# Performance work log

Measured on AMD Instinct MI355X. Metric: run time of the kernel, lower is better.

Reference implementation:

```python
import jax, jax.numpy as jnp
import numpy as np

N = 50000   # nodes
E = 800000  # edges (avg degree 16)
D = 128     # in = hidden = out feats


def setup_inputs() -> dict:
    key = jax.random.key(0)
    ks = jax.random.split(key, 9)
    x = jax.random.normal(ks[0], (N, D), dtype=jnp.float32)
    edge_index = jax.random.randint(ks[1], (2, E), 0, N, dtype=jnp.int64)
    s = 1.0 / np.sqrt(D)
    # SAGEConv layer 0 (128 -> 128): lin_l (aggregated neighbors, with bias), lin_r (root, no bias)
    Wl0 = jax.random.uniform(ks[2], (D, D), jnp.float32, -s, s)
    Wr0 = jax.random.uniform(ks[3], (D, D), jnp.float32, -s, s)
    b0 = jax.random.uniform(ks[4], (D,), jnp.float32, -s, s)
    # SAGEConv layer 1 (128 -> 128)
    Wl1 = jax.random.uniform(ks[5], (D, D), jnp.float32, -s, s)
    Wr1 = jax.random.uniform(ks[6], (D, D), jnp.float32, -s, s)
    b1 = jax.random.uniform(ks[7], (D,), jnp.float32, -s, s)
    return {"x": x, "edge_index": edge_index,
            "Wl0": Wl0, "Wr0": Wr0, "b0": b0,
            "Wl1": Wl1, "Wr1": Wr1, "b1": b1}


def _sage_conv(x, src, dst, Wl, Wr, b):
    # mean aggregation of neighbor messages x[src] into dst nodes
    msgs = x[src]                                                    # [E, D]
    summed = jax.ops.segment_sum(msgs, dst, num_segments=N)         # [N, D]
    deg = jax.ops.segment_sum(jnp.ones((src.shape[0], 1), x.dtype), dst,
                              num_segments=N)                       # [N, 1]
    agg = summed / jnp.maximum(deg, 1.0)
    # out = lin_l(agg) + lin_r(x); only lin_l has bias (PyG default)
    return agg @ Wl.T + b + x @ Wr.T


def reference(x, edge_index, Wl0, Wr0, b0, Wl1, Wr1, b1):
    src, dst = edge_index[0], edge_index[1]
    h = jax.nn.relu(_sage_conv(x, src, dst, Wl0, Wr0, b0))
    out = _sage_conv(h, src, dst, Wl1, Wr1, b1)  # no ReLU on last layer
    return out
```

## Files before the change

### kernel.cpp

```cpp
#include <hip/hip_runtime.h>


#define D 128
#define NBITS 7
#define BNODES 128
#define GA 64
#define AGGB 2048
typedef unsigned short u16;
typedef unsigned u32;
typedef short bf16x8 __attribute__((ext_vector_type(8)));
typedef float f32x4 __attribute__((ext_vector_type(4)));

__device__ __forceinline__ u16 f2bf(float f) {
    union { float f; unsigned u; } x;
    x.f = f;
    unsigned r = x.u + 0x7FFF + ((x.u >> 16) & 1);
    return (u16)(r >> 16);
}
__device__ __forceinline__ float bf2f(u16 b) {
    union { unsigned u; float f; } x;
    x.u = ((unsigned)b) << 16;
    return x.f;
}

__global__ __launch_bounds__(1024) void hist_and_convert(
        const int* __restrict__ dst, int* __restrict__ Gcounts, int E, int NB, int chunk,
        const float* __restrict__ x, u16* __restrict__ xq, int xOcts, int n32,
        const float* __restrict__ w0, const float* __restrict__ w1,
        const float* __restrict__ w2, const float* __restrict__ w3,
        u16* __restrict__ o0, u16* __restrict__ o1,
        u16* __restrict__ o2, u16* __restrict__ o3) {
    if (blockIdx.x < GA) {
        __shared__ int cnt[512];
        for (int i = threadIdx.x; i < NB; i += 1024) cnt[i] = 0;
        __syncthreads();
        int base = blockIdx.x * chunk;
        int end = base + chunk; if (end > E) end = E;
        for (int e = base + threadIdx.x; e < end; e += 1024)
            atomicAdd(&cnt[dst[e] >> NBITS], 1);
        __syncthreads();
        for (int b = threadIdx.x; b < NB; b += 1024)
            Gcounts[b * GA + blockIdx.x] = cnt[b];
    } else {
        int i = (blockIdx.x - GA) * 1024 + threadIdx.x;
        if (i < xOcts) {
            int node = i >> 4;
            int f = (i & 15) * 8;
            int q = f >> 5, off = f & 31;
            float4 va = *(const float4*)&x[node * D + f];
            float4 vb = *(const float4*)&x[node * D + f + 4];
            bf16x8 o;
            o[0] = (short)f2bf(va.x); o[1] = (short)f2bf(va.y);
            o[2] = (short)f2bf(va.z); o[3] = (short)f2bf(va.w);
            o[4] = (short)f2bf(vb.x); o[5] = (short)f2bf(vb.y);
            o[6] = (short)f2bf(vb.z); o[7] = (short)f2bf(vb.w);
            *(bf16x8*)&xq[q * n32 + node * 32 + off] = o;
        } else {
            int j = i - xOcts;
            const int q = D * D / 4;
            if (j < 4 * q) {
                int m = j / q, k = j % q;
                const float* in = (m == 0) ? w0 : (m == 1) ? w1 : (m == 2) ? w2 : w3;
                u16* op = (m == 0) ? o0 : (m == 1) ? o1 : (m == 2) ? o2 : o3;
                float4 v = *(const float4*)&in[k * 4];
                ushort4 o;
                o.x = f2bf(v.x); o.y = f2bf(v.y); o.z = f2bf(v.z); o.w = f2bf(v.w);
                *(ushort4*)&op[k * 4] = o;
            }
        }
    }
}

__global__ __launch_bounds__(1024) void scan1_kernel(const int* __restrict__ in,
                                                     int* __restrict__ excl,
                                                     int* __restrict__ totals, int n) {
    int chunk = blockIdx.x;
    int i = chunk * 1024 + threadIdx.x;
    int v = (i < n) ? in[i] : 0;
    int lane = threadIdx.x & 63;
    int wid = threadIdx.x >> 6;
    int s = v;
    #pragma unroll
    for (int off = 1; off < 64; off <<= 1) {
        int t = __shfl_up(s, off);
        if (lane >= off) s += t;
    }
    __shared__ int wsum[16];
    if (lane == 63) wsum[wid] = s;
    __syncthreads();
    if (wid == 0) {
        int ws = (lane < 16) ? wsum[lane] : 0;
        #pragma unroll
        for (int off = 1; off < 16; off <<= 1) {
            int t = __shfl_up(ws, off);
            if (lane >= off) ws += t;
        }
        if (lane < 16) wsum[lane] = ws;
    }
    __syncthreads();
    int wave_off = (wid > 0) ? wsum[wid - 1] : 0;
    int incl = s + wave_off;
    if (i < n) excl[i] = incl - v;
    if (threadIdx.x == 1023) totals[chunk] = incl;
}

__device__ __forceinline__ void load_choff(const int* __restrict__ totals,
                                           int nChunks, int* choff) {
    if (threadIdx.x < 64) {
        int t = threadIdx.x;
        int v = (t < nChunks) ? totals[t] : 0;
        int s = v;
        #pragma unroll
        for (int off = 1; off < 64; off <<= 1) {
            int u = __shfl_up(s, off);
            if (t >= off) s += u;
        }
        if (t < 32) choff[t] = s - v;
    }
}

__global__ __launch_bounds__(1024) void bucket_scatter(const int* __restrict__ src,
                                                       const int* __restrict__ dst,
                                                       const int* __restrict__ excl,
                                                       const int* __restrict__ totals,
                                                       u32* __restrict__ Ebuck,
                                                       int E, int NB, int chunk, int nChunks) {
    __shared__ int cur[512];
    __shared__ int choff[32];
    load_choff(totals, nChunks, choff);
    __syncthreads();
    for (int b = threadIdx.x; b < NB; b += 1024) {
        int idx = b * GA + blockIdx.x;
        cur[b] = excl[idx] + choff[idx >> 10];
    }
    __syncthreads();
    int base = blockIdx.x * chunk;
    int end = base + chunk; if (end > E) end = E;
    for (int e = base + threadIdx.x; e < end; e += 1024) {
        int d = dst[e];
        int b = d >> NBITS;
        int pos = atomicAdd(&cur[b], 1);
        Ebuck[pos] = ((u32)(d & (BNODES - 1)) << 16) | (u32)src[e];
    }
}

__global__ __launch_bounds__(256) void bucket_sort_csr(const u32* __restrict__ Ebuck,
                                                       const int* __restrict__ excl_g,
                                                       const int* __restrict__ totals,
                                                       int* __restrict__ row_ptr,
                                                       u16* __restrict__ csr,
                                                       int E, int N, int NB, int nChunks) {
    __shared__ int hist[BNODES], excl[BNODES], cur[BNODES];
    __shared__ u16 sorted[8192];
    __shared__ int choff[32];
    load_choff(totals, nChunks, choff);
    __syncthreads();
    int b = blockIdx.x;
    int idx0 = b * GA;
    int start = excl_g[idx0] + choff[idx0 >> 10];
    int endv = E;
    if (b + 1 < NB) {
        int idx1 = (b + 1) * GA;
        endv = excl_g[idx1] + choff[idx1 >> 10];
    }
    int cnt = endv - start;
    if (cnt > 8192) cnt = 8192;
    for (int i = threadIdx.x; i < BNODES; i += 256) hist[i] = 0;
    __syncthreads();
    for (int i = threadIdx.x; i < cnt; i += 256)
        atomicAdd(&hist[Ebuck[start + i] >> 16], 1);
    __syncthreads();
    if (threadIdx.x == 0) {
        int run = 0;
        for (int i = 0; i < BNODES; ++i) { excl[i] = run; run += hist[i]; }
    }
    __syncthreads();
    for (int i = threadIdx.x; i < BNODES; i += 256) {
        cur[i] = excl[i];
        int g = b * BNODES + i;
        if (g <= N) row_ptr[g] = start + excl[i];
    }
    __syncthreads();
    for (int i = threadIdx.x; i < cnt; i += 256) {
        u32 r = Ebuck[start + i];
        int pos = atomicAdd(&cur[r >> 16], 1);
        sorted[pos] = (u16)(r & 0xFFFF);
    }
    __syncthreads();
    for (int i = threadIdx.x; i < cnt; i += 256)
        csr[start + i] = sorted[i];
}

__global__ __launch_bounds__(256) void aggregate_pin(const u16* __restrict__ xq,
                                                     const int* __restrict__ row_ptr,
                                                     const u16* __restrict__ csr,
                                                     u16* __restrict__ aggq,
                                                     int n, int n32, int chunkN) {
    int b = blockIdx.x;
    int strip = b & 3;
    int cid = (b >> 3) * 2 + ((b >> 2) & 1);
    int slot = (threadIdx.x >> 6) * 16 + ((threadIdx.x & 63) >> 2);
    int fl = (threadIdx.x & 3) * 8;
    const u16* __restrict__ base = xq + strip * n32;
    u16* __restrict__ obase = aggq + strip * n32;
    int start = cid * chunkN;
    int endn = start + chunkN; if (endn > n) endn = n;
    for (int node = start + slot; node < endn; node += 64) {
        int begin = row_ptr[node], end = row_ptr[node + 1];
        float a0 = 0.f, a1 = 0.f, a2 = 0.f, a3 = 0.f;
        float a4 = 0.f, a5 = 0.f, a6 = 0.f, a7 = 0.f;
        int j = begin;
        if (j + 3 < end) {
            int s0 = csr[j], s1 = csr[j + 1], s2 = csr[j + 2], s3 = csr[j + 3];
            for (; j + 7 < end; j += 4) {
                int t0 = csr[j + 4], t1 = csr[j + 5], t2 = csr[j + 6], t3 = csr[j + 7];
                bf16x8 v0 = *(const bf16x8*)&base[s0 * 32 + fl];
                bf16x8 v1 = *(const bf16x8*)&base[s1 * 32 + fl];
                bf16x8 v2 = *(const bf16x8*)&base[s2 * 32 + fl];
                bf16x8 v3 = *(const bf16x8*)&base[s3 * 32 + fl];
                a0 += (bf2f((u16)v0[0]) + bf2f((u16)v1[0])) + (bf2f((u16)v2[0]) + bf2f((u16)v3[0]));
                a1 += (bf2f((u16)v0[1]) + bf2f((u16)v1[1])) + (bf2f((u16)v2[1]) + bf2f((u16)v3[1]));
                a2 += (bf2f((u16)v0[2]) + bf2f((u16)v1[2])) + (bf2f((u16)v2[2]) + bf2f((u16)v3[2]));
                a3 += (bf2f((u16)v0[3]) + bf2f((u16)v1[3])) + (bf2f((u16)v2[3]) + bf2f((u16)v3[3]));
                a4 += (bf2f((u16)v0[4]) + bf2f((u16)v1[4])) + (bf2f((u16)v2[4]) + bf2f((u16)v3[4]));
                a5 += (bf2f((u16)v0[5]) + bf2f((u16)v1[5])) + (bf2f((u16)v2[5]) + bf2f((u16)v3[5]));
                a6 += (bf2f((u16)v0[6]) + bf2f((u16)v1[6])) + (bf2f((u16)v2[6]) + bf2f((u16)v3[6]));
                a7 += (bf2f((u16)v0[7]) + bf2f((u16)v1[7])) + (bf2f((u16)v2[7]) + bf2f((u16)v3[7]));
                s0 = t0; s1 = t1; s2 = t2; s3 = t3;
            }
            {
                bf16x8 v0 = *(const bf16x8*)&base[s0 * 32 + fl];
                bf16x8 v1 = *(const bf16x8*)&base[s1 * 32 + fl];
                bf16x8 v2 = *(const bf16x8*)&base[s2 * 32 + fl];
                bf16x8 v3 = *(const bf16x8*)&base[s3 * 32 + fl];
                a0 += (bf2f((u16)v0[0]) + bf2f((u16)v1[0])) + (bf2f((u16)v2[0]) + bf2f((u16)v3[0]));
                a1 += (bf2f((u16)v0[1]) + bf2f((u16)v1[1])) + (bf2f((u16)v2[1]) + bf2f((u16)v3[1]));
                a2 += (bf2f((u16)v0[2]) + bf2f((u16)v1[2])) + (bf2f((u16)v2[2]) + bf2f((u16)v3[2]));
                a3 += (bf2f((u16)v0[3]) + bf2f((u16)v1[3])) + (bf2f((u16)v2[3]) + bf2f((u16)v3[3]));
                a4 += (bf2f((u16)v0[4]) + bf2f((u16)v1[4])) + (bf2f((u16)v2[4]) + bf2f((u16)v3[4]));
                a5 += (bf2f((u16)v0[5]) + bf2f((u16)v1[5])) + (bf2f((u16)v2[5]) + bf2f((u16)v3[5]));
                a6 += (bf2f((u16)v0[6]) + bf2f((u16)v1[6])) + (bf2f((u16)v2[6]) + bf2f((u16)v3[6]));
                a7 += (bf2f((u16)v0[7]) + bf2f((u16)v1[7])) + (bf2f((u16)v2[7]) + bf2f((u16)v3[7]));
                j += 4;
            }
        }
        for (; j < end; ++j) {
            int s0 = csr[j];
            bf16x8 v0 = *(const bf16x8*)&base[s0 * 32 + fl];
            a0 += bf2f((u16)v0[0]); a1 += bf2f((u16)v0[1]);
            a2 += bf2f((u16)v0[2]); a3 += bf2f((u16)v0[3]);
            a4 += bf2f((u16)v0[4]); a5 += bf2f((u16)v0[5]);
            a6 += bf2f((u16)v0[6]); a7 += bf2f((u16)v0[7]);
        }
        int d = end - begin;
        if (d < 1) d = 1;
        float inv = 1.0f / (float)d;
        bf16x8 o;
        o[0] = (short)f2bf(a0 * inv); o[1] = (short)f2bf(a1 * inv);
        o[2] = (short)f2bf(a2 * inv); o[3] = (short)f2bf(a3 * inv);
        o[4] = (short)f2bf(a4 * inv); o[5] = (short)f2bf(a5 * inv);
        o[6] = (short)f2bf(a6 * inv); o[7] = (short)f2bf(a7 * inv);
        *(bf16x8*)&obase[node * 32 + fl] = o;
    }
}

#define LSTR 136

__global__ __launch_bounds__(256) void gemm_mfma(const u16* __restrict__ Aroot,
                                                 const u16* __restrict__ Wr,
                                                 const u16* __restrict__ Agg,
                                                 const u16* __restrict__ Wl,
                                                 const float* __restrict__ bias,
                                                 void* __restrict__ out,
                                                 int n, int n32, int mode) {
    __shared__ __align__(16) u16 Lr[64 * LSTR];
    __shared__ __align__(16) u16 Lg[64 * LSTR];
    const int tid = threadIdx.x;
    const int n0 = blockIdx.x * 64;

    {
        int row = tid >> 4;
        int c = (tid & 15) * 8;
        int q = c >> 5, off = c & 31;
        const u16* ar = Aroot + q * n32;
        const u16* ag = Agg + q * n32;
        #pragma unroll
        for (int p = 0; p < 4; ++p) {
            int r = p * 16 + row;
            int g = n0 + r;
            float4 vr = make_float4(0.f, 0.f, 0.f, 0.f);
            float4 vg = make_float4(0.f, 0.f, 0.f, 0.f);
            if (g < n) {
                vr = *(const float4*)&ar[g * 32 + off];
                vg = *(const float4*)&ag[g * 32 + off];
            }
            *(float4*)&Lr[r * LSTR + c] = vr;
            *(float4*)&Lg[r * LSTR + c] = vg;
        }
    }

    const int wave = tid >> 6;
    const int lane = tid & 63;
    const int quad = lane >> 4;
    const int l16 = lane & 15;

    bf16x8 wr[2][4], wl[2][4];
    #pragma unroll
    for (int mt = 0; mt < 2; ++mt) {
        int jrow = wave * 32 + mt * 16 + l16;
        #pragma unroll
        for (int kb = 0; kb < 4; ++kb) {
            wr[mt][kb] = *(const bf16x8*)&Wr[jrow * D + kb * 32 + quad * 8];
            wl[mt][kb] = *(const bf16x8*)&Wl[jrow * D + kb * 32 + quad * 8];
        }
    }

    __syncthreads();

    f32x4 acc[4][2];
    #pragma unroll
    for (int it = 0; it < 4; ++it)
        #pragma unroll
        for (int mt = 0; mt < 2; ++mt)
            acc[it][mt] = (f32x4){0.f, 0.f, 0.f, 0.f};

    #pragma unroll
    for (int it = 0; it < 4; ++it) {
        int base = (it * 16 + l16) * LSTR + quad * 8;
        #pragma unroll
        for (int kb = 0; kb < 4; ++kb) {
            bf16x8 bx = *(const bf16x8*)&Lr[base + kb * 32];
            bf16x8 bg = *(const bf16x8*)&Lg[base + kb * 32];
            #pragma unroll
            for (int mt = 0; mt < 2; ++mt) {
                acc[it][mt] = __builtin_amdgcn_mfma_f32_16x16x32_bf16(wr[mt][kb], bx, acc[it][mt], 0, 0, 0);
                acc[it][mt] = __builtin_amdgcn_mfma_f32_16x16x32_bf16(wl[mt][kb], bg, acc[it][mt], 0, 0, 0);
            }
        }
    }

    #pragma unroll
    for (int it = 0; it < 4; ++it) {
        int i = n0 + it * 16 + l16;
        if (i < n) {
            #pragma unroll
            for (int mt = 0; mt < 2; ++mt) {
                int j0 = wave * 32 + mt * 16 + quad * 4;
                float4 bv = *(const float4*)&bias[j0];
                float o0 = acc[it][mt][0] + bv.x;
                float o1 = acc[it][mt][1] + bv.y;
                float o2 = acc[it][mt][2] + bv.z;
                float o3 = acc[it][mt][3] + bv.w;
                if (mode) {
                    o0 = fmaxf(o0, 0.f); o1 = fmaxf(o1, 0.f);
                    o2 = fmaxf(o2, 0.f); o3 = fmaxf(o3, 0.f);
                    ushort4 ob;
                    ob.x = f2bf(o0); ob.y = f2bf(o1); ob.z = f2bf(o2); ob.w = f2bf(o3);
                    int jj = mt * 16 + quad * 4;
                    *(ushort4*)&((u16*)out)[wave * n32 + i * 32 + jj] = ob;
                } else {
                    float4 of = make_float4(o0, o1, o2, o3);
                    *(float4*)&((float*)out)[i * D + j0] = of;
                }
            }
        }
    }
}


extern "C" void kernel_launch(void* const* d_in, const int* in_sizes, int n_in,
                              void* d_out, int out_size, void* d_ws, size_t ws_size,
                              hipStream_t stream) {
    const float* x = (const float*)d_in[0];
    const int* edge = (const int*)d_in[1];
    const float* Wl0 = (const float*)d_in[2];
    const float* Wr0 = (const float*)d_in[3];
    const float* b0 = (const float*)d_in[4];
    const float* Wl1 = (const float*)d_in[5];
    const float* Wr1 = (const float*)d_in[6];
    const float* b1 = (const float*)d_in[7];

    const int N = in_sizes[0] / D;
    const int E = in_sizes[1] / 2;
    const int* src = edge;
    const int* dst = edge + E;

    char* ws = (char*)d_ws;
    size_t off = 0;
    auto alloc = [&](size_t bytes) {
        char* p = ws + off;
        off += (bytes + 255) & ~(size_t)255;
        return p;
    };
    int* row_ptr = (int*)alloc((size_t)(N + 1) * 4);
    u32* Ebuck = (u32*)alloc((size_t)E * 4);
    u16* csrb = (u16*)alloc((size_t)E * 2);
    u16* xq = (u16*)alloc((size_t)N * D * 2);
    u16* hq = (u16*)alloc((size_t)N * D * 2);
    u16* aggq = (u16*)alloc((size_t)N * D * 2);
    u16* Wl0b = (u16*)alloc((size_t)D * D * 2);
    u16* Wr0b = (u16*)alloc((size_t)D * D * 2);
    u16* Wl1b = (u16*)alloc((size_t)D * D * 2);
    u16* Wr1b = (u16*)alloc((size_t)D * D * 2);
    const int NB = (N + BNODES - 1) / BNODES;
    const int scanN = NB * GA;
    int* Gcounts = (int*)alloc((size_t)scanN * 4);
    int* Sc = (int*)alloc((size_t)scanN * 4);
    int* totals = (int*)alloc(32 * 4);

    (void)ws_size; (void)n_in; (void)out_size;

    const int chunk = (E + GA - 1) / GA;
    const int n32 = N * 32;
    const int xOcts = N * D / 8;
    const int convThreads = xOcts + 4 * D * D / 4;
    const int histGrid = GA + (convThreads + 1023) / 1024;
    const int nChunks = (scanN + 1023) / 1024;
    const int chunkN = (N + 511) / 512;
    const int gemmBlocks = (N + 63) / 64;

    hist_and_convert<<<histGrid, 1024, 0, stream>>>(
        dst, Gcounts, E, NB, chunk,
        x, xq, xOcts, n32,
        Wl0, Wr0, Wl1, Wr1, Wl0b, Wr0b, Wl1b, Wr1b);
    scan1_kernel<<<nChunks, 1024, 0, stream>>>(Gcounts, Sc, totals, scanN);
    bucket_scatter<<<GA, 1024, 0, stream>>>(src, dst, Sc, totals, Ebuck, E, NB, chunk, nChunks);
    bucket_sort_csr<<<NB, 256, 0, stream>>>(Ebuck, Sc, totals, row_ptr, csrb, E, N, NB, nChunks);

    aggregate_pin<<<AGGB, 256, 0, stream>>>(xq, row_ptr, csrb, aggq, N, n32, chunkN);
    gemm_mfma<<<gemmBlocks, 256, 0, stream>>>(xq, Wr0b, aggq, Wl0b, b0, hq, N, n32, 1);
    aggregate_pin<<<AGGB, 256, 0, stream>>>(hq, row_ptr, csrb, aggq, N, n32, chunkN);
    gemm_mfma<<<gemmBlocks, 256, 0, stream>>>(hq, Wr1b, aggq, Wl1b, b1, d_out, N, n32, 0);
}
```

Baseline: 201.9 us.

## Sort nodes by in-degree so aggregation wavefronts get balanced work

```diff
diff --git a/kernel.cpp b/kernel.cpp
--- a/kernel.cpp
+++ b/kernel.cpp
@@ -149,11 +149,14 @@
                                                        const int* __restrict__ totals,
                                                        int* __restrict__ row_ptr,
                                                        u16* __restrict__ csr,
+                                                       int* __restrict__ DegCounts,
                                                        int E, int N, int NB, int nChunks) {
     __shared__ int hist[BNODES], excl[BNODES], cur[BNODES];
     __shared__ u16 sorted[8192];
     __shared__ int choff[32];
+    __shared__ int degh[64];
     load_choff(totals, nChunks, choff);
+    for (int i = threadIdx.x; i < 64; i += 256) degh[i] = 0;
     __syncthreads();
     int b = blockIdx.x;
     int idx0 = b * GA;
@@ -174,12 +177,22 @@
         int run = 0;
         for (int i = 0; i < BNODES; ++i) { excl[i] = run; run += hist[i]; }
     }
+    for (int i = threadIdx.x; i < BNODES; i += 256) {
+        int g = b * BNODES + i;
+        if (g < N) {
+            int dg = hist[i];
+            if (dg > 63) dg = 63;
+            atomicAdd(&degh[dg], 1);
+        }
+    }
     __syncthreads();
     for (int i = threadIdx.x; i < BNODES; i += 256) {
         cur[i] = excl[i];
         int g = b * BNODES + i;
         if (g <= N) row_ptr[g] = start + excl[i];
     }
+    for (int i = threadIdx.x; i < 64; i += 256)
+        DegCounts[i * NB + b] = degh[i];
     __syncthreads();
     for (int i = threadIdx.x; i < cnt; i += 256) {
         u32 r = Ebuck[start + i];
@@ -191,9 +204,37 @@
         csr[start + i] = sorted[i];
 }
 
+__global__ __launch_bounds__(128) void deg_scatter(const int* __restrict__ row_ptr,
+                                                   const int* __restrict__ SdC,
+                                                   const int* __restrict__ totals2,
+                                                   u16* __restrict__ order,
+                                                   int N, int NB, int nChunks2) {
+    __shared__ int choff[32];
+    __shared__ int cur[64];
+    load_choff(totals2, nChunks2, choff);
+    __syncthreads();
+    int b = blockIdx.x;
+    for (int d = threadIdx.x; d < 64; d += 128) {
+        int idx = d * NB + b;
+        cur[d] = SdC[idx] + choff[idx >> 10];
+    }
+    __syncthreads();
+    int i = threadIdx.x;
+    if (i < BNODES) {
+        int g = b * BNODES + i;
+        if (g < N) {
+            int dg = row_ptr[g + 1] - row_ptr[g];
+            if (dg > 63) dg = 63;
+            int pos = atomicAdd(&cur[dg], 1);
+            order[pos] = (u16)g;
+        }
+    }
+}
+
 __global__ __launch_bounds__(256) void aggregate_pin(const u16* __restrict__ xq,
                                                      const int* __restrict__ row_ptr,
                                                      const u16* __restrict__ csr,
+                                                     const u16* __restrict__ order,
                                                      u16* __restrict__ aggq,
                                                      int n, int n32, int chunkN) {
     int b = blockIdx.x;
@@ -205,7 +246,8 @@
     u16* __restrict__ obase = aggq + strip * n32;
     int start = cid * chunkN;
     int endn = start + chunkN; if (endn > n) endn = n;
-    for (int node = start + slot; node < endn; node += 64) {
+    for (int idx = start + slot; idx < endn; idx += 64) {
+        int node = order[idx];
         int begin = row_ptr[node], end = row_ptr[node + 1];
         float a0 = 0.f, a1 = 0.f, a2 = 0.f, a3 = 0.f;
         float a4 = 0.f, a5 = 0.f, a6 = 0.f, a7 = 0.f;
@@ -407,6 +449,10 @@
     int* Gcounts = (int*)alloc((size_t)scanN * 4);
     int* Sc = (int*)alloc((size_t)scanN * 4);
     int* totals = (int*)alloc(32 * 4);
+    int* DegCounts = (int*)alloc((size_t)scanN * 4);
+    int* SdC = (int*)alloc((size_t)scanN * 4);
+    int* totals2 = (int*)alloc(32 * 4);
+    u16* order = (u16*)alloc((size_t)N * 2);
 
     (void)ws_size; (void)n_in; (void)out_size;
 
@@ -425,10 +471,13 @@
         Wl0, Wr0, Wl1, Wr1, Wl0b, Wr0b, Wl1b, Wr1b);
     scan1_kernel<<<nChunks, 1024, 0, stream>>>(Gcounts, Sc, totals, scanN);
     bucket_scatter<<<GA, 1024, 0, stream>>>(src, dst, Sc, totals, Ebuck, E, NB, chunk, nChunks);
-    bucket_sort_csr<<<NB, 256, 0, stream>>>(Ebuck, Sc, totals, row_ptr, csrb, E, N, NB, nChunks);
-
-    aggregate_pin<<<AGGB, 256, 0, stream>>>(xq, row_ptr, csrb, aggq, N, n32, chunkN);
+    bucket_sort_csr<<<NB, 256, 0, stream>>>(Ebuck, Sc, totals, row_ptr, csrb, DegCounts, E, N, NB, nChunks);
+
+    scan1_kernel<<<nChunks, 1024, 0, stream>>>(DegCounts, SdC, totals2, scanN);
+    deg_scatter<<<NB, 128, 0, stream>>>(row_ptr, SdC, totals2, order, N, NB, nChunks);
+
+    aggregate_pin<<<AGGB, 256, 0, stream>>>(xq, row_ptr, csrb, order, aggq, N, n32, chunkN);
     gemm_mfma<<<gemmBlocks, 256, 0, stream>>>(xq, Wr0b, aggq, Wl0b, b0, hq, N, n32, 1);
-    aggregate_pin<<<AGGB, 256, 0, stream>>>(hq, row_ptr, csrb, aggq, N, n32, chunkN);
+    aggregate_pin<<<AGGB, 256, 0, stream>>>(hq, row_ptr, csrb, order, aggq, N, n32, chunkN);
     gemm_mfma<<<gemmBlocks, 256, 0, stream>>>(hq, Wr1b, aggq, Wl1b, b1, d_out, N, n32, 0);
 }
```

After: 219.2 us. 8.6% more time.
